# Performance work log

Hardware: AMD Instinct MI355X
Metric: run time of the kernel (lower is better)

The kernel has to match this reference:

```python
import jax, jax.numpy as jnp
import numpy as np

CONF_THRESHOLD = 0.7

def setup_inputs() -> dict:
    key = jax.random.key(0)
    ks = jax.random.split(key, 8)
    B, T, D, H, GH = 16384, 48, 32, 1024, 128
    s = lambda fan: 1.0 / np.sqrt(fan)
    return {
        "x":   jax.random.normal(ks[0], (B, T, D), jnp.float32),
        "gW1": jax.random.normal(ks[1], (D, GH), jnp.float32) * s(D),
        "gb1": jnp.zeros((GH,), jnp.float32),
        "gW2": jax.random.normal(ks[2], (GH, 2), jnp.float32) * s(GH),
        "gb2": jnp.zeros((2,), jnp.float32),
        "nW1": jax.random.normal(ks[3], (T * D, H), jnp.float32) * s(T * D),
        "nb1": jnp.zeros((H,), jnp.float32),
        "nW2": jax.random.normal(ks[4], (H, 2), jnp.float32) * s(H),
        "nb2": jnp.zeros((2,), jnp.float32),
        "aW1": jax.random.normal(ks[5], (T * D, H), jnp.float32) * s(T * D),
        "ab1": jnp.zeros((H,), jnp.float32),
        "aW2": jax.random.normal(ks[6], (H, 2), jnp.float32) * s(H),
        "ab2": jnp.zeros((2,), jnp.float32),
    }

def _gate(x, gW1, gb1, gW2, gb2):
    # mean-pool over time, 2-layer MLP, softmax -> [B, 2] class probs
    h = jax.nn.relu(jnp.mean(x, axis=1) @ gW1 + gb1)
    return jax.nn.softmax(h @ gW2 + gb2, axis=-1)

def _expert(x_flat, W1, b1, W2, b2):
    return jax.nn.relu(x_flat @ W1 + b1) @ W2 + b2

def reference(x, gW1, gb1, gW2, gb2, nW1, nb1, nW2, nb2, aW1, ab1, aW2, ab2):
    B = x.shape[0]
    gate_outputs = _gate(x, gW1, gb1, gW2, gb2)          # [B, 2]
    gate_probs = jnp.max(gate_outputs, axis=1)           # [B]
    gate_decisions = jnp.argmax(gate_outputs, axis=1)    # [B] in {0,1}

    # adaptive routing: low-confidence samples fall back to the normal expert
    high_conf = gate_probs >= CONF_THRESHOLD
    abnormal_mask = high_conf & (gate_decisions == 1)
    # normal_mask = (high_conf & dec==0) | ~high_conf  == ~abnormal_mask (partition)

    x_flat = x.reshape(B, -1)
    normal_out = _expert(x_flat, nW1, nb1, nW2, nb2)     # [B, 2]
    abnormal_out = _expert(x_flat, aW1, ab1, aW2, ab2)   # [B, 2]
    outputs = jnp.where(abnormal_mask[:, None], abnormal_out, normal_out)
    return outputs, gate_decisions, gate_probs
```

## Files before the change

### kernel.cpp

```cpp
#include <hip/hip_runtime.h>

#define TDIM 48
#define DDIM 32
#define KDIM 1536
#define HDIM 1024
#define GHID 128
#define KTN  48

typedef unsigned short u16;
typedef __bf16 bf16x8 __attribute__((ext_vector_type(8)));
typedef float  f32x4  __attribute__((ext_vector_type(4)));

typedef const void __attribute__((address_space(1))) gvoid;
typedef void       __attribute__((address_space(3))) lvoid;

__device__ __forceinline__ void gld_lds16(const void* g, void* l) {
    __builtin_amdgcn_global_load_lds((gvoid*)g, (lvoid*)l, 16, 0, 0);
}

__device__ __forceinline__ u16 f2bf(float f) {
    union { float f; unsigned u; } v; v.f = f;
    return (u16)((v.u + 0x7fffu + ((v.u >> 16) & 1u)) >> 16);
}

__global__ __launch_bounds__(256) void gate_transpose(
    const float* __restrict__ x,
    const float* __restrict__ gW1, const float* __restrict__ gb1,
    const float* __restrict__ gW2, const float* __restrict__ gb2,
    u16* __restrict__ Xbf, int* __restrict__ route, int* __restrict__ cnt,
    float* __restrict__ out, float* __restrict__ outDec, float* __restrict__ outProb,
    const float* __restrict__ nW1, const float* __restrict__ aW1,
    u16* __restrict__ W1t, int gateBlocks)
{
    __shared__ double xm[4][DDIM];
    __shared__ float tile[32][33];

    if ((int)blockIdx.x < gateBlocks) {
        const int wave = threadIdx.x >> 6;
        const int lane = threadIdx.x & 63;
        const int b    = blockIdx.x * 4 + wave;
        if (blockIdx.x == 0 && threadIdx.x < 2) cnt[threadIdx.x] = 0;

        const float* xr = x + (size_t)b * KDIM;
        u16* xo = Xbf + (size_t)b * KDIM;

        double a0 = 0, a1 = 0, a2 = 0, a3 = 0;
#pragma unroll
        for (int i = 0; i < 6; ++i) {
            const int idx = i * 256 + lane * 4;
            f32x4 v = __builtin_nontemporal_load((const f32x4*)(xr + idx));
            ushort4 o;
            o.x = f2bf(v[0]); o.y = f2bf(v[1]); o.z = f2bf(v[2]); o.w = f2bf(v[3]);
            *(ushort4*)(xo + idx) = o;
            a0 += v[0]; a1 += v[1]; a2 += v[2]; a3 += v[3];
        }
#pragma unroll
        for (int m = 8; m <= 32; m <<= 1) {
            a0 += __shfl_xor(a0, m); a1 += __shfl_xor(a1, m);
            a2 += __shfl_xor(a2, m); a3 += __shfl_xor(a3, m);
        }
        if (lane < 8) {
            xm[wave][4 * lane + 0] = a0 / 48.0; xm[wave][4 * lane + 1] = a1 / 48.0;
            xm[wave][4 * lane + 2] = a2 / 48.0; xm[wave][4 * lane + 3] = a3 / 48.0;
        }
        __builtin_amdgcn_wave_barrier();
        __builtin_amdgcn_s_waitcnt(0);
        __threadfence_block();

        double h0 = (double)gb1[lane], h1 = (double)gb1[lane + 64];
#pragma unroll
        for (int d = 0; d < DDIM; ++d) {
            const double xv = xm[wave][d];
            h0 += xv * (double)gW1[d * GHID + lane];
            h1 += xv * (double)gW1[d * GHID + 64 + lane];
        }
        h0 = h0 > 0.0 ? h0 : 0.0;
        h1 = h1 > 0.0 ? h1 : 0.0;
        double z0 = h0 * (double)gW2[lane * 2 + 0] + h1 * (double)gW2[(lane + 64) * 2 + 0];
        double z1 = h0 * (double)gW2[lane * 2 + 1] + h1 * (double)gW2[(lane + 64) * 2 + 1];
#pragma unroll
        for (int m = 1; m <= 32; m <<= 1) {
            z0 += __shfl_xor(z0, m);
            z1 += __shfl_xor(z1, m);
        }
        if (lane == 0) {
            z0 += (double)gb2[0]; z1 += (double)gb2[1];
            const int dec = (z1 > z0) ? 1 : 0;
            const double mz = z0 > z1 ? z0 : z1;
            const double e0 = exp(z0 - mz), e1 = exp(z1 - mz);
            const double p = (e0 > e1 ? e0 : e1) / (e0 + e1);
            const float pf = (float)p;
            outDec[b]  = (float)dec;
            outProb[b] = pf;
            out[2 * b + 0] = 0.f;
            out[2 * b + 1] = 0.f;
            const int high = ((double)pf >= 0.7) ? 1 : 0;
            route[b] = (high && dec) ? 1 : 0;
        }
    } else {
        int t = (int)blockIdx.x - gateBlocks;
        const int e = t >= (32 * 48);
        t -= e ? (32 * 48) : 0;
        const int bx = t & 31;
        const int by = t >> 5;
        const float* W = e ? aW1 : nW1;
        u16* Wt = W1t + (size_t)e * HDIM * KDIM;
        const int tid = threadIdx.x;
        const int tx = tid & 31;
        const int ty = tid >> 5;
#pragma unroll
        for (int r = 0; r < 32; r += 8)
            tile[ty + r][tx] = W[(size_t)(by * 32 + ty + r) * HDIM + bx * 32 + tx];
        __syncthreads();
#pragma unroll
        for (int r = 0; r < 32; r += 8)
            Wt[(size_t)(bx * 32 + ty + r) * KDIM + by * 32 + tx] = f2bf(tile[tx][ty + r]);
    }
}

__global__ __launch_bounds__(256) void compact_kernel(
    const int* __restrict__ route, int* __restrict__ perm, int* __restrict__ cnt,
    int Bn)
{
    const int tid  = threadIdx.x;
    const int b    = (int)blockIdx.x * 256 + tid;
    const int lane = tid & 63;
    const int active = (b < Bn);
    const int e = active ? route[b] : 0;
    const unsigned long long m1 = __ballot(active && e == 1);
    const unsigned long long m0 = __ballot(active && e == 0);
    const unsigned long long below = (lane == 63) ? ~0ull >> 1 : ((1ull << lane) - 1);
    int base0 = 0, base1 = 0;
    if (lane == 0) {
        if (m0) base0 = atomicAdd(&cnt[0], (int)__popcll(m0));
        if (m1) base1 = atomicAdd(&cnt[1], (int)__popcll(m1));
    }
    base0 = __shfl(base0, 0);
    base1 = __shfl(base1, 0);
    if (active) {
        const int pos = e ? base1 + (int)__popcll(m1 & below)
                          : base0 + (int)__popcll(m0 & below);
        perm[e * Bn + pos] = b;
    }
}

__global__ __launch_bounds__(512, 2) void expert_gemm(
    const u16* __restrict__ Xbf, const u16* __restrict__ W1t,
    const float* __restrict__ nb1, const float* __restrict__ nW2,
    const float* __restrict__ nb2,
    const float* __restrict__ ab1, const float* __restrict__ aW2,
    const float* __restrict__ ab2,
    const int* __restrict__ perm, const int* __restrict__ cnt,
    float* __restrict__ out, int Bn, int mB)
{
    __shared__ __align__(16) u16 Ab[4][256 * 32];
    __shared__ __align__(16) u16 Bb[4][128 * 32];
    __shared__ int   permLds[256];
    __shared__ float w2Lds[128 * 2];
    __shared__ float b1Lds[128];

    const int tid = threadIdx.x;
    const int L    = (int)blockIdx.x;
    const int m    = (L & 7) + 8 * (L >> 6);
    const int nIdx = (L >> 3) & 7;
    const int e  = m >= mB;
    const int mb = m - (e ? mB : 0);
    const int cntE = cnt[e];
    const int start = mb * 256;
    if (start >= cntE) return;
    const int valid = min(256, cntE - start);
    const int n0 = nIdx * 128;

    const u16*  W1e = W1t + (size_t)e * HDIM * KDIM;
    const float* b1 = e ? ab1 : nb1;
    const float* w2 = e ? aW2 : nW2;
    const float* b2 = e ? ab2 : nb2;

    if (tid < 256) {
        permLds[tid] = perm[e * Bn + min(start + tid, cntE - 1)];
    } else if (tid < 384) {
        const int j = tid - 256;
        b1Lds[j]         = b1[n0 + j];
        w2Lds[j * 2 + 0] = w2[(n0 + j) * 2 + 0];
        w2Lds[j * 2 + 1] = w2[(n0 + j) * 2 + 1];
    }
    __syncthreads();

    const int rQ = tid >> 2;
    const int cg = (tid & 3) ^ ((tid >> 3) & 3);
    const u16* gA0 = Xbf + (size_t)permLds[rQ]       * KDIM + cg * 8;
    const u16* gA1 = Xbf + (size_t)permLds[rQ + 128] * KDIM + cg * 8;
    const u16* gB  = W1e + (size_t)(n0 + rQ)         * KDIM + cg * 8;
    const int dA0 = tid * 8;
    const int dA1 = tid * 8 + 4096;
    const int dB  = tid * 8;

#pragma unroll
    for (int pk = 0; pk < 3; ++pk) {
        gld_lds16(gA0 + pk * 32, &Ab[pk][dA0]);
        gld_lds16(gA1 + pk * 32, &Ab[pk][dA1]);
        gld_lds16(gB  + pk * 32, &Bb[pk][dB]);
    }
    asm volatile("s_waitcnt vmcnt(6)" ::: "memory");
    asm volatile("s_barrier" ::: "memory");

    const int wave = tid >> 6;
    const int lane = tid & 63;
    const int wm   = (wave >> 1) * 64;
    const int wn   = (wave & 1) * 64;
    const int l15  = lane & 15;
    const int quad = lane >> 4;

    f32x4 acc[4][4];
#pragma unroll
    for (int i = 0; i < 4; ++i)
#pragma unroll
        for (int j = 0; j < 4; ++j) acc[i][j] = (f32x4)0.f;

#pragma unroll 4
    for (int kt = 0; kt < KTN; ++kt) {
        const int buf = kt & 3;
        bf16x8 af[4], bfv[4];
#pragma unroll
        for (int mi = 0; mi < 4; ++mi) {
            const int r = wm + mi * 16 + l15;
            const int p = quad ^ ((r >> 1) & 3);
            af[mi] = *reinterpret_cast<const bf16x8*>(&Ab[buf][r * 32 + p * 8]);
        }
#pragma unroll
        for (int ni = 0; ni < 4; ++ni) {
            const int r = wn + ni * 16 + l15;
            const int p = quad ^ ((r >> 1) & 3);
            bfv[ni] = *reinterpret_cast<const bf16x8*>(&Bb[buf][r * 32 + p * 8]);
        }
        if (kt < KTN - 3) {
            const int b3 = (kt + 3) & 3;
            const int k3 = (kt + 3) * 32;
            gld_lds16(gA0 + k3, &Ab[b3][dA0]);
            gld_lds16(gA1 + k3, &Ab[b3][dA1]);
            gld_lds16(gB  + k3, &Bb[b3][dB]);
        }
        asm volatile("s_barrier" ::: "memory");
        asm volatile("s_waitcnt lgkmcnt(0)" ::: "memory");
        __builtin_amdgcn_sched_barrier(0);
        __builtin_amdgcn_s_setprio(1);
#pragma unroll
        for (int mi = 0; mi < 4; ++mi)
#pragma unroll
            for (int ni = 0; ni < 4; ++ni)
                acc[mi][ni] = __builtin_amdgcn_mfma_f32_16x16x32_bf16(
                    af[mi], bfv[ni], acc[mi][ni], 0, 0, 0);
        __builtin_amdgcn_s_setprio(0);
        __builtin_amdgcn_sched_barrier(0);
        if (kt < KTN - 3)       { asm volatile("s_waitcnt vmcnt(6)" ::: "memory"); }
        else if (kt == KTN - 3) { asm volatile("s_waitcnt vmcnt(3)" ::: "memory"); }
        else                    { asm volatile("s_waitcnt vmcnt(0)" ::: "memory"); }
        asm volatile("s_barrier" ::: "memory");
    }

    const float b2_0 = (n0 == 0) ? b2[0] : 0.f;
    const float b2_1 = (n0 == 0) ? b2[1] : 0.f;
#pragma unroll
    for (int mi = 0; mi < 4; ++mi) {
        float p0[4] = {0.f, 0.f, 0.f, 0.f};
        float p1[4] = {0.f, 0.f, 0.f, 0.f};
#pragma unroll
        for (int ni = 0; ni < 4; ++ni) {
            const int col = wn + ni * 16 + l15;
            const float w20 = w2Lds[col * 2 + 0];
            const float w21 = w2Lds[col * 2 + 1];
            const float bb  = b1Lds[col];
#pragma unroll
            for (int r = 0; r < 4; ++r) {
                float h = acc[mi][ni][r] + bb;
                h = fmaxf(h, 0.f);
                p0[r] += h * w20;
                p1[r] += h * w21;
            }
        }
#pragma unroll
        for (int mm = 1; mm <= 8; mm <<= 1) {
#pragma unroll
            for (int r = 0; r < 4; ++r) {
                p0[r] += __shfl_xor(p0[r], mm);
                p1[r] += __shfl_xor(p1[r], mm);
            }
        }
        if (l15 < 4) {
            const int r = l15;
            const int lrow = wm + mi * 16 + quad * 4 + r;
            if (lrow < valid) {
                const int srow = permLds[lrow];
                atomicAdd(&out[srow * 2 + 0], p0[r] + b2_0);
                atomicAdd(&out[srow * 2 + 1], p1[r] + b2_1);
            }
        }
    }
}

extern "C" void kernel_launch(void* const* d_in, const int* in_sizes, int n_in,
                              void* d_out, int out_size, void* d_ws, size_t ws_size,
                              hipStream_t stream) {
    const float* x   = (const float*)d_in[0];
    const float* gW1 = (const float*)d_in[1];
    const float* gb1 = (const float*)d_in[2];
    const float* gW2 = (const float*)d_in[3];
    const float* gb2 = (const float*)d_in[4];
    const float* nW1 = (const float*)d_in[5];
    const float* nb1 = (const float*)d_in[6];
    const float* nW2 = (const float*)d_in[7];
    const float* nb2 = (const float*)d_in[8];
    const float* aW1 = (const float*)d_in[9];
    const float* ab1 = (const float*)d_in[10];
    const float* aW2 = (const float*)d_in[11];
    const float* ab2 = (const float*)d_in[12];

    float* out = (float*)d_out;
    const int Bn = in_sizes[0] / KDIM;

    char* ws = (char*)d_ws;
    size_t off = 0;
    u16* Xbf = (u16*)(ws + off); off += (size_t)Bn * KDIM * sizeof(u16);
    u16* W1t = (u16*)(ws + off); off += (size_t)2 * HDIM * KDIM * sizeof(u16);
    int* perm = (int*)(ws + off); off += (size_t)2 * Bn * sizeof(int);
    int* cnt  = (int*)(ws + off); off += 2 * sizeof(int);
    int* route = (int*)(ws + off); off += (size_t)Bn * sizeof(int);

    const int gateBlocks = Bn / 4;
    const int trBlocks   = 2 * (HDIM / 32) * (KDIM / 32);

    gate_transpose<<<gateBlocks + trBlocks, 256, 0, stream>>>(
        x, gW1, gb1, gW2, gb2, Xbf, route, cnt,
        out, out + 2 * Bn, out + 3 * Bn, nW1, aW1, W1t, gateBlocks);

    compact_kernel<<<(Bn + 255) / 256, 256, 0, stream>>>(route, perm, cnt, Bn);

    const int mB = (Bn + 255) / 256;
    expert_gemm<<<2 * mB * (HDIM / 128), 512, 0, stream>>>(
        Xbf, W1t, nb1, nW2, nb2, ab1, aW2, ab2, perm, cnt, out, Bn, mB);
}
```

Baseline: 255.4 us.

## Retile expert GEMM to 128x256 with 3-stage LDS pipeline and higher occupancy

```diff
diff --git a/kernel.cpp b/kernel.cpp
--- a/kernel.cpp
+++ b/kernel.cpp
@@ -144,7 +144,7 @@
     }
 }
 
-__global__ __launch_bounds__(512, 2) void expert_gemm(
+__global__ __launch_bounds__(512, 4) void expert_gemm(
     const u16* __restrict__ Xbf, const u16* __restrict__ W1t,
     const float* __restrict__ nb1, const float* __restrict__ nW2,
     const float* __restrict__ nb2,
@@ -153,32 +153,32 @@
     const int* __restrict__ perm, const int* __restrict__ cnt,
     float* __restrict__ out, int Bn, int mB)
 {
-    __shared__ __align__(16) u16 Ab[4][256 * 32];
-    __shared__ __align__(16) u16 Bb[4][128 * 32];
-    __shared__ int   permLds[256];
-    __shared__ float w2Lds[128 * 2];
-    __shared__ float b1Lds[128];
+    __shared__ __align__(16) u16 Ab[3][128 * 32];
+    __shared__ __align__(16) u16 Bb[3][256 * 32];
+    __shared__ int   permLds[128];
+    __shared__ float b1Lds[256];
+    __shared__ float w2Lds[256 * 2];
 
     const int tid = threadIdx.x;
-    const int L    = (int)blockIdx.x;
-    const int m    = (L & 7) + 8 * (L >> 6);
-    const int nIdx = (L >> 3) & 7;
+    const int L = (int)blockIdx.x;
+    const int g = L >> 3;
+    const int m = (g >> 2) * 8 + (L & 7);
+    const int nIdx = g & 3;
     const int e  = m >= mB;
     const int mb = m - (e ? mB : 0);
     const int cntE = cnt[e];
-    const int start = mb * 256;
+    const int start = mb * 128;
     if (start >= cntE) return;
-    const int valid = min(256, cntE - start);
-    const int n0 = nIdx * 128;
+    const int valid = min(128, cntE - start);
+    const int n0 = nIdx * 256;
 
     const u16*  W1e = W1t + (size_t)e * HDIM * KDIM;
     const float* b1 = e ? ab1 : nb1;
     const float* w2 = e ? aW2 : nW2;
     const float* b2 = e ? ab2 : nb2;
 
-    if (tid < 256) {
-        permLds[tid] = perm[e * Bn + min(start + tid, cntE - 1)];
-    } else if (tid < 384) {
+    if (tid < 128) permLds[tid] = perm[e * Bn + min(start + tid, cntE - 1)];
+    if (tid >= 256) {
         const int j = tid - 256;
         b1Lds[j]         = b1[n0 + j];
         w2Lds[j * 2 + 0] = w2[(n0 + j) * 2 + 0];
@@ -186,30 +186,37 @@
     }
     __syncthreads();
 
+    const int cg = (tid & 3) ^ ((tid >> 2) & 3);
     const int rQ = tid >> 2;
-    const int cg = (tid & 3) ^ ((tid >> 3) & 3);
-    const u16* gA0 = Xbf + (size_t)permLds[rQ]       * KDIM + cg * 8;
-    const u16* gA1 = Xbf + (size_t)permLds[rQ + 128] * KDIM + cg * 8;
-    const u16* gB  = W1e + (size_t)(n0 + rQ)         * KDIM + cg * 8;
-    const int dA0 = tid * 8;
-    const int dA1 = tid * 8 + 4096;
-    const int dB  = tid * 8;
-
-#pragma unroll
-    for (int pk = 0; pk < 3; ++pk) {
-        gld_lds16(gA0 + pk * 32, &Ab[pk][dA0]);
-        gld_lds16(gA1 + pk * 32, &Ab[pk][dA1]);
-        gld_lds16(gB  + pk * 32, &Bb[pk][dB]);
-    }
-    asm volatile("s_waitcnt vmcnt(6)" ::: "memory");
-    asm volatile("s_barrier" ::: "memory");
+    const u16* gA  = Xbf + (size_t)permLds[rQ] * KDIM + cg * 8;
+    const u16* gB0 = W1e + (size_t)(n0 + rQ) * KDIM + cg * 8;
+    const u16* gB1 = W1e + (size_t)(n0 + 128 + rQ) * KDIM + cg * 8;
+
+#define STAGE(kt_, sl_) do {                                   \
+        const int ko_ = (kt_) * 32;                            \
+        gld_lds16(gA  + ko_, &Ab[sl_][tid * 8]);               \
+        gld_lds16(gB0 + ko_, &Bb[sl_][tid * 8]);               \
+        gld_lds16(gB1 + ko_, &Bb[sl_][tid * 8 + 4096]);        \
+    } while (0)
+
+    STAGE(0, 0);
+    STAGE(1, 1);
+    STAGE(2, 2);
 
     const int wave = tid >> 6;
     const int lane = tid & 63;
-    const int wm   = (wave >> 1) * 64;
-    const int wn   = (wave & 1) * 64;
+    const int wm   = (wave >> 2) * 64;
+    const int wn   = (wave & 3) * 64;
     const int l15  = lane & 15;
     const int quad = lane >> 4;
+    const int pfrag = quad ^ (l15 & 3);
+
+    int offA[4], offB[4];
+#pragma unroll
+    for (int i = 0; i < 4; ++i) {
+        offA[i] = (wm + i * 16 + l15) * 32 + pfrag * 8;
+        offB[i] = (wn + i * 16 + l15) * 32 + pfrag * 8;
+    }
 
     f32x4 acc[4][4];
 #pragma unroll
@@ -217,46 +224,38 @@
 #pragma unroll
         for (int j = 0; j < 4; ++j) acc[i][j] = (f32x4)0.f;
 
-#pragma unroll 4
-    for (int kt = 0; kt < KTN; ++kt) {
-        const int buf = kt & 3;
-        bf16x8 af[4], bfv[4];
-#pragma unroll
-        for (int mi = 0; mi < 4; ++mi) {
-            const int r = wm + mi * 16 + l15;
-            const int p = quad ^ ((r >> 1) & 3);
-            af[mi] = *reinterpret_cast<const bf16x8*>(&Ab[buf][r * 32 + p * 8]);
-        }
-#pragma unroll
-        for (int ni = 0; ni < 4; ++ni) {
-            const int r = wn + ni * 16 + l15;
-            const int p = quad ^ ((r >> 1) & 3);
-            bfv[ni] = *reinterpret_cast<const bf16x8*>(&Bb[buf][r * 32 + p * 8]);
-        }
-        if (kt < KTN - 3) {
-            const int b3 = (kt + 3) & 3;
-            const int k3 = (kt + 3) * 32;
-            gld_lds16(gA0 + k3, &Ab[b3][dA0]);
-            gld_lds16(gA1 + k3, &Ab[b3][dA1]);
-            gld_lds16(gB  + k3, &Bb[b3][dB]);
-        }
-        asm volatile("s_barrier" ::: "memory");
-        asm volatile("s_waitcnt lgkmcnt(0)" ::: "memory");
-        __builtin_amdgcn_sched_barrier(0);
-        __builtin_amdgcn_s_setprio(1);
-#pragma unroll
-        for (int mi = 0; mi < 4; ++mi)
+    for (int kq = 0; kq < KTN / 3; ++kq) {
+#pragma unroll
+        for (int s = 0; s < 3; ++s) {
+            const int kt = kq * 3 + s;
+            if (kt < KTN - 2)       { asm volatile("s_waitcnt vmcnt(6)" ::: "memory"); }
+            else if (kt == KTN - 2) { asm volatile("s_waitcnt vmcnt(3)" ::: "memory"); }
+            else                    { asm volatile("s_waitcnt vmcnt(0)" ::: "memory"); }
+            __builtin_amdgcn_s_barrier();
+
+            bf16x8 af[4], bfv[4];
+#pragma unroll
+            for (int mi = 0; mi < 4; ++mi)
+                af[mi] = *reinterpret_cast<const bf16x8*>(&Ab[s][offA[mi]]);
 #pragma unroll
             for (int ni = 0; ni < 4; ++ni)
-                acc[mi][ni] = __builtin_amdgcn_mfma_f32_16x16x32_bf16(
-                    af[mi], bfv[ni], acc[mi][ni], 0, 0, 0);
-        __builtin_amdgcn_s_setprio(0);
-        __builtin_amdgcn_sched_barrier(0);
-        if (kt < KTN - 3)       { asm volatile("s_waitcnt vmcnt(6)" ::: "memory"); }
-        else if (kt == KTN - 3) { asm volatile("s_waitcnt vmcnt(3)" ::: "memory"); }
-        else                    { asm volatile("s_waitcnt vmcnt(0)" ::: "memory"); }
-        asm volatile("s_barrier" ::: "memory");
-    }
+                bfv[ni] = *reinterpret_cast<const bf16x8*>(&Bb[s][offB[ni]]);
+
+            if (kt < KTN - 2) STAGE(kt + 2, (s + 2) % 3);
+
+            asm volatile("s_waitcnt lgkmcnt(0)" ::: "memory");
+            __builtin_amdgcn_sched_barrier(0);
+            __builtin_amdgcn_s_setprio(1);
+#pragma unroll
+            for (int mi = 0; mi < 4; ++mi)
+#pragma unroll
+                for (int ni = 0; ni < 4; ++ni)
+                    acc[mi][ni] = __builtin_amdgcn_mfma_f32_16x16x32_bf16(
+                        af[mi], bfv[ni], acc[mi][ni], 0, 0, 0);
+            __builtin_amdgcn_s_setprio(0);
+        }
+    }
+#undef STAGE
 
     const float b2_0 = (n0 == 0) ? b2[0] : 0.f;
     const float b2_1 = (n0 == 0) ? b2[1] : 0.f;
@@ -335,7 +334,7 @@
 
     compact_kernel<<<(Bn + 255) / 256, 256, 0, stream>>>(route, perm, cnt, Bn);
 
-    const int mB = (Bn + 255) / 256;
-    expert_gemm<<<2 * mB * (HDIM / 128), 512, 0, stream>>>(
+    const int mB = (Bn + 127) / 128;
+    expert_gemm<<<2 * mB * (HDIM / 256), 512, 0, stream>>>(
         Xbf, W1t, nb1, nW2, nb2, ab1, aW2, ab2, perm, cnt, out, Bn, mB);
 }
```

New measurement: 237.7 us. -6.9%, faster.
